# Optimization experiments

Measured on AMD Instinct MI355X. Metric: run time of the kernel, lower is better.

The kernel has to match this reference:

```python
import jax, jax.numpy as jnp
import numpy as np

ALPHA = 0.2
BETA = 1.0
TEMPERATURE = 0.05
EPS = 1e-8  # torch cosine_similarity eps


def setup_inputs() -> dict:
    key = jax.random.key(0)
    k1, k2 = jax.random.split(key)
    B, R, D = 4096, 18, 256  # rows, segment size (1 anchor + 1 pos + 16 negs), embed dim
    features = jax.random.normal(k1, (B * R, D), dtype=jnp.float32)
    scores = jax.random.normal(k2, (B * (R - 1),), dtype=jnp.float32)
    row_sizes = jnp.full((B,), R, dtype=jnp.int32)  # uniform ragged sizes
    logit_scale = jnp.array([1.0 / TEMPERATURE], dtype=jnp.float32)
    return {"features": features, "scores": scores, "row_sizes": row_sizes,
            "logit_scale": logit_scale}


def reference(features, scores, row_sizes, logit_scale):
    B = row_sizes.shape[0]
    R = features.shape[0] // B  # uniform segment size
    D = features.shape[1]
    f3 = features.reshape(B, R, D)
    anchor = f3[:, 0]          # [B, D]
    tgt = f3[:, 1:]            # [B, R-1, D]  (positive first, then negatives)

    # --- per-row cosine sims + log_softmax + KLDiv(batchmean) ---
    an = jnp.maximum(jnp.linalg.norm(anchor, axis=-1, keepdims=True), EPS)  # [B,1]
    tn = jnp.maximum(jnp.linalg.norm(tgt, axis=-1), EPS)                    # [B,R-1]
    cos = jnp.einsum('bd,bkd->bk', anchor, tgt) / (an * tn)                 # [B,R-1]
    emb_log = jax.nn.log_softmax(cos, axis=-1)                              # [B,R-1]
    ce = jax.nn.softmax(scores.reshape(B, R - 1), axis=-1)                  # [B,R-1]
    # torch KLDivLoss(reduction='batchmean') on a length-(R-1) vector divides by (R-1)
    kl = jnp.sum(ce * (jnp.log(ce) - emb_log), axis=-1) / (R - 1)           # [B]
    loss = jnp.mean(BETA * kl)

    # --- single InfoNCE over all rows: anchors vs [positives; all negatives] ---
    pos = f3[:, 1]                                   # [B, D]
    negs = f3[:, 2:].reshape(B * (R - 2), D)         # [B*(R-2), D]
    targets = jnp.concatenate([pos, negs], axis=0)   # [B*(R-1), D]
    logits = logit_scale[0] * (anchor @ targets.T)   # [B, B*(R-1)]
    labels = jnp.arange(B)
    # cross_entropy(logits, labels) with mean reduction
    infonce = jnp.mean(jax.nn.logsumexp(logits, axis=-1) - logits[labels, labels])

    return loss + ALPHA * infonce
```

## Files before the change

### kernel.cpp

```cpp
#include <hip/hip_runtime.h>
#include <math.h>

#define ALPHA 0.2f
#define BETA 1.0f
#define EPSV 1e-8f
#define LOG2E 1.4426950408889634f
#define LN2 0.6931471805599453f

#define BATCH 4096
#define RR 18
#define KT 17
#define DD 256
#define NTGT (BATCH*KT)

#define BMW 64
#define NWAVES 4
#define BMB (BMW*NWAVES)
#define MBLK (BATCH/BMB)
#define BN 64
#define NSPLIT 32
#define NSLOT (NSPLIT*2)
#define NSLICE (NTGT/NSPLIT)
#define NCHUNK (NSLICE/BN)
#define CHUNK_BYTES (BN*DD)
#define TSH_STRIDE 272

typedef int   i32x8  __attribute__((ext_vector_type(8)));
typedef float f32x16 __attribute__((ext_vector_type(16)));

__device__ inline void gl_lds16(const void* g, void* l){
  __builtin_amdgcn_global_load_lds(
      (const __attribute__((address_space(1))) unsigned int*)g,
      (__attribute__((address_space(3))) unsigned int*)l, 16, 0, 0);
}


__global__ __launch_bounds__(256) void prep_kernel(
    const float* __restrict__ feat, const float* __restrict__ scores,
    const float* __restrict__ lscale,
    unsigned char* __restrict__ abf8, unsigned char* __restrict__ tbf8,
    float* __restrict__ diag, float* __restrict__ klarr){
  __shared__ float csh[KT];
  __shared__ __align__(16) unsigned char tsh[KT*TSH_STRIDE];
  int b = blockIdx.x, tid = threadIdx.x, lane = tid & 63, wave = tid >> 6;
  const float* fb = feat + (size_t)b * RR * DD;
  float s2 = lscale[0] * LOG2E;

  float4 a4 = ((const float4*)fb)[lane];
  float asq = a4.x*a4.x + a4.y*a4.y + a4.z*a4.z + a4.w*a4.w;
  #pragma unroll
  for (int off=1; off<64; off<<=1) asq += __shfl_xor(asq, off);
  float an = fmaxf(sqrtf(asq), EPSV);

  if (wave == 0){
    int p = __builtin_amdgcn_cvt_pk_fp8_f32(a4.x*s2, a4.y*s2, 0, false);
    p     = __builtin_amdgcn_cvt_pk_fp8_f32(a4.z*s2, a4.w*s2, p, true);
    *(int*)(abf8 + (size_t)b*DD + lane*4) = p;
  }

  for (int kr = wave+1; kr <= KT; kr += NWAVES){
    float4 t4 = ((const float4*)(fb + (size_t)kr*DD))[lane];
    int p = __builtin_amdgcn_cvt_pk_fp8_f32(t4.x, t4.y, 0, false);
    p     = __builtin_amdgcn_cvt_pk_fp8_f32(t4.z, t4.w, p, true);
    *(int*)&tsh[(kr-1)*TSH_STRIDE + lane*4] = p;
    float d = a4.x*t4.x + a4.y*t4.y + a4.z*t4.z + a4.w*t4.w;
    float q = t4.x*t4.x + t4.y*t4.y + t4.z*t4.z + t4.w*t4.w;
    #pragma unroll
    for (int off=1; off<64; off<<=1){ d += __shfl_xor(d,off); q += __shfl_xor(q,off); }
    if (lane == 0){
      csh[kr-1] = d / (an * fmaxf(sqrtf(q), EPSV));
      if (kr == 1) diag[b] = d;
    }
  }
  __syncthreads();

  for (int idx = tid; idx < KT*16; idx += 256){
    int g = idx / KT;
    int j = idx - g*KT;
    int ki = g >> 2, half = (g >> 1) & 1, w = g & 1;
    int t  = b*KT + j;
    int c  = t >> 6, r = t & 63, mt = (r >> 5) & 1, m = r & 31;
    uint4 v = *(const uint4*)&tsh[j*TSH_STRIDE + ki*64 + half*32 + w*16];
    size_t dst = (size_t)c*CHUNK_BYTES + (size_t)((ki*2+mt)*2 + w)*1024
               + half*512 + m*16;
    *(uint4*)(tbf8 + dst) = v;
  }

  if (tid == 0){
    float cm = -INFINITY;
    #pragma unroll
    for (int j=0;j<KT;++j) cm = fmaxf(cm, csh[j]);
    float cs = 0.f;
    #pragma unroll
    for (int j=0;j<KT;++j) cs += __builtin_amdgcn_exp2f((csh[j]-cm)*LOG2E);
    float lse_c = cm + __logf(cs);

    const float* sb = scores + (size_t)b*KT;
    float sv[KT];
    #pragma unroll
    for (int j=0;j<KT;++j) sv[j] = sb[j];
    float sm = -INFINITY;
    #pragma unroll
    for (int j=0;j<KT;++j) sm = fmaxf(sm, sv[j]);
    float ss = 0.f;
    #pragma unroll
    for (int j=0;j<KT;++j) ss += __builtin_amdgcn_exp2f((sv[j]-sm)*LOG2E);
    float lse_s = sm + __logf(ss);

    float kl = 0.f;
    #pragma unroll
    for (int j=0;j<KT;++j){
      float lq = sv[j]  - lse_s;
      float lp = csh[j] - lse_c;
      kl += __builtin_amdgcn_exp2f(lq*LOG2E)*(lq - lp);
    }
    klarr[b] = kl * (1.0f/KT);
  }
}

__global__ __launch_bounds__(256,2) void gemm_lse_kernel(
    const unsigned char* __restrict__ abf8, const unsigned char* __restrict__ tbf8,
    float* __restrict__ part_m, float* __restrict__ part_s){
  __shared__ __align__(16) unsigned char Bs[2][CHUNK_BYTES];
  const int tid  = threadIdx.x;
  const int lane = tid & 63;
  const int wave = tid >> 6;
  const int mb   = blockIdx.y;
  const int ns   = blockIdx.x;
  const int l31  = lane & 31;
  const int half = lane >> 5;

  const char* gbase = (const char*)tbf8 + (size_t)(ns*NCHUNK)*CHUNK_BYTES;
  auto stage = [&](int ch){
    const char* g = gbase + (size_t)ch*CHUNK_BYTES;
    char* l = (char*)Bs[ch & 1];
    #pragma unroll
    for (int j=0;j<4;++j){
      int off = j*4096 + tid*16;
      gl_lds16(g + off, l + off);
    }
  };

  stage(0);

  i32x8 af[2][4];
  {
    const unsigned char* ab = abf8 + (size_t)(mb*BMB + wave*BMW)*DD;
    #pragma unroll
    for (int nt=0;nt<2;++nt)
      #pragma unroll
      for (int ki=0;ki<4;++ki){
        const unsigned char* p = ab + (size_t)(nt*32+l31)*DD + ki*64 + half*32;
        uint4 lo = *(const uint4*)p;
        uint4 hi = *(const uint4*)(p+16);
        af[nt][ki] = (i32x8){(int)lo.x,(int)lo.y,(int)lo.z,(int)lo.w,
                             (int)hi.x,(int)hi.y,(int)hi.z,(int)hi.w};
      }
  }

  float run_m[2] = {-INFINITY,-INFINITY};
  float run_s[2] = {0.f,0.f};

  for (int ch=0; ch<NCHUNK; ++ch){
    __syncthreads();
    if (ch+1 < NCHUNK) stage(ch+1);

    const unsigned char* frag = &Bs[ch & 1][0] + lane*16;

    f32x16 acc[2][2];
    #pragma unroll
    for (int mt=0;mt<2;++mt)
      #pragma unroll
      for (int nt=0;nt<2;++nt)
        acc[mt][nt] = (f32x16)(0.f);

    #pragma unroll
    for (int ki=0;ki<4;++ki){
      i32x8 tf[2];
      #pragma unroll
      for (int mt=0;mt<2;++mt){
        uint4 lo = *(const uint4*)(frag + (size_t)((ki*2+mt)*2+0)*1024);
        uint4 hi = *(const uint4*)(frag + (size_t)((ki*2+mt)*2+1)*1024);
        tf[mt] = (i32x8){(int)lo.x,(int)lo.y,(int)lo.z,(int)lo.w,
                         (int)hi.x,(int)hi.y,(int)hi.z,(int)hi.w};
      }
      acc[0][0] = __builtin_amdgcn_mfma_scale_f32_32x32x64_f8f6f4(
                      tf[0], af[0][ki], acc[0][0], 0,0, 0,127, 0,127);
      acc[0][1] = __builtin_amdgcn_mfma_scale_f32_32x32x64_f8f6f4(
                      tf[0], af[1][ki], acc[0][1], 0,0, 0,127, 0,127);
      acc[1][0] = __builtin_amdgcn_mfma_scale_f32_32x32x64_f8f6f4(
                      tf[1], af[0][ki], acc[1][0], 0,0, 0,127, 0,127);
      acc[1][1] = __builtin_amdgcn_mfma_scale_f32_32x32x64_f8f6f4(
                      tf[1], af[1][ki], acc[1][1], 0,0, 0,127, 0,127);
    }

    #pragma unroll
    for (int nt=0;nt<2;++nt){
      f32x16 t = __builtin_elementwise_max(acc[0][nt], acc[1][nt]);
      float m8[8];
      #pragma unroll
      for (int i=0;i<8;++i) m8[i] = fmaxf(t[i], t[i+8]);
      float m4a = fmaxf(m8[0],m8[1]), m4b = fmaxf(m8[2],m8[3]);
      float m4c = fmaxf(m8[4],m8[5]), m4d = fmaxf(m8[6],m8[7]);
      float mx = fmaxf(fmaxf(m4a,m4b), fmaxf(m4c,m4d));

      float s0=0.f, s1=0.f, s2=0.f, s3=0.f;
      #pragma unroll
      for (int r=0;r<16;r+=4){
        s0 += __builtin_amdgcn_exp2f(acc[0][nt][r  ]-mx) + __builtin_amdgcn_exp2f(acc[1][nt][r  ]-mx);
        s1 += __builtin_amdgcn_exp2f(acc[0][nt][r+1]-mx) + __builtin_amdgcn_exp2f(acc[1][nt][r+1]-mx);
        s2 += __builtin_amdgcn_exp2f(acc[0][nt][r+2]-mx) + __builtin_amdgcn_exp2f(acc[1][nt][r+2]-mx);
        s3 += __builtin_amdgcn_exp2f(acc[0][nt][r+3]-mx) + __builtin_amdgcn_exp2f(acc[1][nt][r+3]-mx);
      }
      float sh = (s0+s1)+(s2+s3);

      float nm = fmaxf(run_m[nt], mx);
      run_s[nt] = run_s[nt]*__builtin_amdgcn_exp2f(run_m[nt]-nm)
                + sh*__builtin_amdgcn_exp2f(mx-nm);
      run_m[nt] = nm;
    }
  }

  #pragma unroll
  for (int nt=0;nt<2;++nt){
    int gm = mb*BMB + wave*BMW + nt*32 + l31;
    int slot = ns*2 + half;
    part_m[(size_t)gm*NSLOT + slot] = run_m[nt];
    part_s[(size_t)gm*NSLOT + slot] = run_s[nt];
  }
}

__global__ __launch_bounds__(256) void combine_kernel(
    const float* __restrict__ part_m, const float* __restrict__ part_s,
    const float* __restrict__ diag, const float* __restrict__ klarr,
    const float* __restrict__ lscale, float* __restrict__ accs){
  int b = blockIdx.x*256 + threadIdx.x;
  float s = lscale[0];
  const float* pm = part_m + (size_t)b*NSLOT;
  const float* ps = part_s + (size_t)b*NSLOT;
  float M = -INFINITY;
  #pragma unroll 8
  for (int i=0;i<NSLOT;++i) M = fmaxf(M, pm[i]);
  float S = 0.f;
  #pragma unroll 8
  for (int i=0;i<NSLOT;++i) S += ps[i]*__builtin_amdgcn_exp2f(pm[i]-M);
  float inf = (M + __log2f(S))*LN2 - s*diag[b];
  float kl  = klarr[b];
  #pragma unroll
  for (int off=1; off<64; off<<=1){
    inf += __shfl_xor(inf, off);
    kl  += __shfl_xor(kl,  off);
  }
  if ((threadIdx.x & 63)==0){
    atomicAdd(accs+1, inf);
    atomicAdd(accs+0, kl);
  }
}

__global__ void final_kernel(const float* __restrict__ accs, float* __restrict__ out){
  out[0] = BETA*(accs[0]*(1.0f/BATCH)) + ALPHA*(accs[1]*(1.0f/BATCH));
}

extern "C" void kernel_launch(void* const* d_in, const int* in_sizes, int n_in,
                              void* d_out, int out_size, void* d_ws, size_t ws_size,
                              hipStream_t stream){
  const float* feat   = (const float*)d_in[0];
  const float* scores = (const float*)d_in[1];
  const float* lscale = (const float*)d_in[3];

  float* ws     = (float*)d_ws;
  float* diag   = ws;
  float* klarr  = diag + BATCH;
  float* part_m = klarr + BATCH;
  float* part_s = part_m + (size_t)BATCH*NSLOT;
  float* accs   = part_s + (size_t)BATCH*NSLOT;
  unsigned char* abf8 = (unsigned char*)(accs + 4);
  unsigned char* tbf8 = abf8 + (size_t)BATCH*DD;

  hipMemsetAsync(accs, 0, 2*sizeof(float), stream);
  prep_kernel<<<BATCH, 256, 0, stream>>>(feat, scores, lscale, abf8, tbf8, diag, klarr);
  gemm_lse_kernel<<<dim3(NSPLIT, MBLK), 256, 0, stream>>>(abf8, tbf8, part_m, part_s);
  combine_kernel<<<BATCH/256, 256, 0, stream>>>(part_m, part_s, diag, klarr, lscale, accs);
  final_kernel<<<1,1,0,stream>>>(accs, (float*)d_out);
}
```

Before: 216.6 us.

## Double GEMM split, drop LDS transpose in prep, wave-per-row combine, deterministic final reduce

The number of target-dimension splits in the fused GEMM+logsumexp kernel doubles to 64 and its occupancy hint rises to 3 blocks per CU, so the 16-row-block grid exposes more parallelism. The prep kernel now gives each 16-lane group one target row and writes the swizzled fp8 layout straight to global memory, dropping the shared-memory staging buffer and its extra pass. The combine step uses one wave per row with shuffle reductions over the larger set of partials, and a single-block final kernel replaces the memset and atomics. The risks are register pressure under the tighter launch bound and twice as much partial data for combine to read.

Measured after the change: 198.6 us. 8.3% less time.

```diff
diff --git a/kernel.cpp b/kernel.cpp
--- a/kernel.cpp
+++ b/kernel.cpp
@@ -18,12 +18,11 @@
 #define BMB (BMW*NWAVES)
 #define MBLK (BATCH/BMB)
 #define BN 64
-#define NSPLIT 32
+#define NSPLIT 64
 #define NSLOT (NSPLIT*2)
 #define NSLICE (NTGT/NSPLIT)
 #define NCHUNK (NSLICE/BN)
 #define CHUNK_BYTES (BN*DD)
-#define TSH_STRIDE 272
 
 typedef int   i32x8  __attribute__((ext_vector_type(8)));
 typedef float f32x16 __attribute__((ext_vector_type(16)));
@@ -32,6 +31,11 @@
   __builtin_amdgcn_global_load_lds(
       (const __attribute__((address_space(1))) unsigned int*)g,
       (__attribute__((address_space(3))) unsigned int*)l, 16, 0, 0);
+}
+
+__device__ inline int pk8(float a, float b, float c, float d){
+  int p = __builtin_amdgcn_cvt_pk_fp8_f32(a, b, 0, false);
+  return  __builtin_amdgcn_cvt_pk_fp8_f32(c, d, p, true);
 }
 
 
@@ -41,84 +45,93 @@
     unsigned char* __restrict__ abf8, unsigned char* __restrict__ tbf8,
     float* __restrict__ diag, float* __restrict__ klarr){
   __shared__ float csh[KT];
-  __shared__ __align__(16) unsigned char tsh[KT*TSH_STRIDE];
-  int b = blockIdx.x, tid = threadIdx.x, lane = tid & 63, wave = tid >> 6;
+  int b = blockIdx.x, tid = threadIdx.x;
+  int grp = tid >> 4, j = tid & 15;
   const float* fb = feat + (size_t)b * RR * DD;
   float s2 = lscale[0] * LOG2E;
 
-  float4 a4 = ((const float4*)fb)[lane];
-  float asq = a4.x*a4.x + a4.y*a4.y + a4.z*a4.z + a4.w*a4.w;
-  #pragma unroll
-  for (int off=1; off<64; off<<=1) asq += __shfl_xor(asq, off);
+  float4 a0 = ((const float4*)fb)[j*4+0];
+  float4 a1 = ((const float4*)fb)[j*4+1];
+  float4 a2 = ((const float4*)fb)[j*4+2];
+  float4 a3 = ((const float4*)fb)[j*4+3];
+  float asq = (a0.x*a0.x+a0.y*a0.y+a0.z*a0.z+a0.w*a0.w)
+            + (a1.x*a1.x+a1.y*a1.y+a1.z*a1.z+a1.w*a1.w)
+            + (a2.x*a2.x+a2.y*a2.y+a2.z*a2.z+a2.w*a2.w)
+            + (a3.x*a3.x+a3.y*a3.y+a3.z*a3.z+a3.w*a3.w);
+  #pragma unroll
+  for (int off=1; off<16; off<<=1) asq += __shfl_xor(asq, off);
   float an = fmaxf(sqrtf(asq), EPSV);
 
-  if (wave == 0){
-    int p = __builtin_amdgcn_cvt_pk_fp8_f32(a4.x*s2, a4.y*s2, 0, false);
-    p     = __builtin_amdgcn_cvt_pk_fp8_f32(a4.z*s2, a4.w*s2, p, true);
-    *(int*)(abf8 + (size_t)b*DD + lane*4) = p;
-  }
-
-  for (int kr = wave+1; kr <= KT; kr += NWAVES){
-    float4 t4 = ((const float4*)(fb + (size_t)kr*DD))[lane];
-    int p = __builtin_amdgcn_cvt_pk_fp8_f32(t4.x, t4.y, 0, false);
-    p     = __builtin_amdgcn_cvt_pk_fp8_f32(t4.z, t4.w, p, true);
-    *(int*)&tsh[(kr-1)*TSH_STRIDE + lane*4] = p;
-    float d = a4.x*t4.x + a4.y*t4.y + a4.z*t4.z + a4.w*t4.w;
-    float q = t4.x*t4.x + t4.y*t4.y + t4.z*t4.z + t4.w*t4.w;
-    #pragma unroll
-    for (int off=1; off<64; off<<=1){ d += __shfl_xor(d,off); q += __shfl_xor(q,off); }
-    if (lane == 0){
+  if (tid < 16){
+    uint4 v = make_uint4(
+      (unsigned)pk8(a0.x*s2,a0.y*s2,a0.z*s2,a0.w*s2),
+      (unsigned)pk8(a1.x*s2,a1.y*s2,a1.z*s2,a1.w*s2),
+      (unsigned)pk8(a2.x*s2,a2.y*s2,a2.z*s2,a2.w*s2),
+      (unsigned)pk8(a3.x*s2,a3.y*s2,a3.z*s2,a3.w*s2));
+    *(uint4*)(abf8 + (size_t)b*DD + j*16) = v;
+  }
+
+  for (int kr = grp+1; kr <= KT; kr += 16){
+    const float4* tp = (const float4*)(fb + (size_t)kr*DD) + j*4;
+    float4 t0=tp[0], t1=tp[1], t2=tp[2], t3=tp[3];
+    int t  = b*KT + (kr-1);
+    int c  = t >> 6, r = t & 63, mt = (r >> 5) & 1, m = r & 31;
+    int ki = j >> 2, hf = (j >> 1) & 1, w = j & 1;
+    uint4 v = make_uint4(
+      (unsigned)pk8(t0.x,t0.y,t0.z,t0.w), (unsigned)pk8(t1.x,t1.y,t1.z,t1.w),
+      (unsigned)pk8(t2.x,t2.y,t2.z,t2.w), (unsigned)pk8(t3.x,t3.y,t3.z,t3.w));
+    *(uint4*)(tbf8 + (size_t)c*CHUNK_BYTES + (size_t)((ki*2+mt)*2+w)*1024
+              + hf*512 + m*16) = v;
+    float d = (a0.x*t0.x+a0.y*t0.y+a0.z*t0.z+a0.w*t0.w)
+            + (a1.x*t1.x+a1.y*t1.y+a1.z*t1.z+a1.w*t1.w)
+            + (a2.x*t2.x+a2.y*t2.y+a2.z*t2.z+a2.w*t2.w)
+            + (a3.x*t3.x+a3.y*t3.y+a3.z*t3.z+a3.w*t3.w);
+    float q = (t0.x*t0.x+t0.y*t0.y+t0.z*t0.z+t0.w*t0.w)
+            + (t1.x*t1.x+t1.y*t1.y+t1.z*t1.z+t1.w*t1.w)
+            + (t2.x*t2.x+t2.y*t2.y+t2.z*t2.z+t2.w*t2.w)
+            + (t3.x*t3.x+t3.y*t3.y+t3.z*t3.z+t3.w*t3.w);
+    #pragma unroll
+    for (int off=1; off<16; off<<=1){ d += __shfl_xor(d,off); q += __shfl_xor(q,off); }
+    if (j == 0){
       csh[kr-1] = d / (an * fmaxf(sqrtf(q), EPSV));
       if (kr == 1) diag[b] = d;
     }
   }
   __syncthreads();
 
-  for (int idx = tid; idx < KT*16; idx += 256){
-    int g = idx / KT;
-    int j = idx - g*KT;
-    int ki = g >> 2, half = (g >> 1) & 1, w = g & 1;
-    int t  = b*KT + j;
-    int c  = t >> 6, r = t & 63, mt = (r >> 5) & 1, m = r & 31;
-    uint4 v = *(const uint4*)&tsh[j*TSH_STRIDE + ki*64 + half*32 + w*16];
-    size_t dst = (size_t)c*CHUNK_BYTES + (size_t)((ki*2+mt)*2 + w)*1024
-               + half*512 + m*16;
-    *(uint4*)(tbf8 + dst) = v;
-  }
-
   if (tid == 0){
     float cm = -INFINITY;
     #pragma unroll
-    for (int j=0;j<KT;++j) cm = fmaxf(cm, csh[j]);
+    for (int i=0;i<KT;++i) cm = fmaxf(cm, csh[i]);
     float cs = 0.f;
     #pragma unroll
-    for (int j=0;j<KT;++j) cs += __builtin_amdgcn_exp2f((csh[j]-cm)*LOG2E);
+    for (int i=0;i<KT;++i) cs += __builtin_amdgcn_exp2f((csh[i]-cm)*LOG2E);
     float lse_c = cm + __logf(cs);
 
     const float* sb = scores + (size_t)b*KT;
     float sv[KT];
     #pragma unroll
-    for (int j=0;j<KT;++j) sv[j] = sb[j];
+    for (int i=0;i<KT;++i) sv[i] = sb[i];
     float sm = -INFINITY;
     #pragma unroll
-    for (int j=0;j<KT;++j) sm = fmaxf(sm, sv[j]);
+    for (int i=0;i<KT;++i) sm = fmaxf(sm, sv[i]);
     float ss = 0.f;
     #pragma unroll
-    for (int j=0;j<KT;++j) ss += __builtin_amdgcn_exp2f((sv[j]-sm)*LOG2E);
+    for (int i=0;i<KT;++i) ss += __builtin_amdgcn_exp2f((sv[i]-sm)*LOG2E);
     float lse_s = sm + __logf(ss);
 
     float kl = 0.f;
     #pragma unroll
-    for (int j=0;j<KT;++j){
-      float lq = sv[j]  - lse_s;
-      float lp = csh[j] - lse_c;
+    for (int i=0;i<KT;++i){
+      float lq = sv[i]  - lse_s;
+      float lp = csh[i] - lse_c;
       kl += __builtin_amdgcn_exp2f(lq*LOG2E)*(lq - lp);
     }
     klarr[b] = kl * (1.0f/KT);
   }
 }
 
-__global__ __launch_bounds__(256,2) void gemm_lse_kernel(
+__global__ __launch_bounds__(256,3) void gemm_lse_kernel(
     const unsigned char* __restrict__ abf8, const unsigned char* __restrict__ tbf8,
     float* __restrict__ part_m, float* __restrict__ part_s){
   __shared__ __align__(16) unsigned char Bs[2][CHUNK_BYTES];
@@ -232,33 +245,44 @@
 
 __global__ __launch_bounds__(256) void combine_kernel(
     const float* __restrict__ part_m, const float* __restrict__ part_s,
-    const float* __restrict__ diag, const float* __restrict__ klarr,
-    const float* __restrict__ lscale, float* __restrict__ accs){
-  int b = blockIdx.x*256 + threadIdx.x;
+    const float* __restrict__ diag, const float* __restrict__ lscale,
+    float* __restrict__ infarr){
+  int lane = threadIdx.x & 63, wave = threadIdx.x >> 6;
+  int b = blockIdx.x*4 + wave;
   float s = lscale[0];
   const float* pm = part_m + (size_t)b*NSLOT;
   const float* ps = part_s + (size_t)b*NSLOT;
-  float M = -INFINITY;
-  #pragma unroll 8
-  for (int i=0;i<NSLOT;++i) M = fmaxf(M, pm[i]);
-  float S = 0.f;
-  #pragma unroll 8
-  for (int i=0;i<NSLOT;++i) S += ps[i]*__builtin_amdgcn_exp2f(pm[i]-M);
-  float inf = (M + __log2f(S))*LN2 - s*diag[b];
-  float kl  = klarr[b];
+  float m0 = pm[lane], m1 = pm[lane+64];
+  float v0 = ps[lane], v1 = ps[lane+64];
+  float M = fmaxf(m0, m1);
+  #pragma unroll
+  for (int off=1; off<64; off<<=1) M = fmaxf(M, __shfl_xor(M, off));
+  float S = v0*__builtin_amdgcn_exp2f(m0-M) + v1*__builtin_amdgcn_exp2f(m1-M);
+  #pragma unroll
+  for (int off=1; off<64; off<<=1) S += __shfl_xor(S, off);
+  if (lane == 0)
+    infarr[b] = (M + __log2f(S))*LN2 - s*diag[b];
+}
+
+__global__ __launch_bounds__(256) void final_kernel(
+    const float* __restrict__ infarr, const float* __restrict__ klarr,
+    float* __restrict__ out){
+  __shared__ float shi[4], shk[4];
+  int tid = threadIdx.x, lane = tid & 63, wave = tid >> 6;
+  float inf = 0.f, kl = 0.f;
+  for (int i = tid; i < BATCH; i += 256){ inf += infarr[i]; kl += klarr[i]; }
   #pragma unroll
   for (int off=1; off<64; off<<=1){
     inf += __shfl_xor(inf, off);
     kl  += __shfl_xor(kl,  off);
   }
-  if ((threadIdx.x & 63)==0){
-    atomicAdd(accs+1, inf);
-    atomicAdd(accs+0, kl);
-  }
-}
-
-__global__ void final_kernel(const float* __restrict__ accs, float* __restrict__ out){
-  out[0] = BETA*(accs[0]*(1.0f/BATCH)) + ALPHA*(accs[1]*(1.0f/BATCH));
+  if (lane == 0){ shi[wave] = inf; shk[wave] = kl; }
+  __syncthreads();
+  if (tid == 0){
+    float I = shi[0]+shi[1]+shi[2]+shi[3];
+    float K = shk[0]+shk[1]+shk[2]+shk[3];
+    out[0] = BETA*(K*(1.0f/BATCH)) + ALPHA*(I*(1.0f/BATCH));
+  }
 }
 
 extern "C" void kernel_launch(void* const* d_in, const int* in_sizes, int n_in,
@@ -271,15 +295,14 @@
   float* ws     = (float*)d_ws;
   float* diag   = ws;
   float* klarr  = diag + BATCH;
-  float* part_m = klarr + BATCH;
+  float* infarr = klarr + BATCH;
+  float* part_m = infarr + BATCH;
   float* part_s = part_m + (size_t)BATCH*NSLOT;
-  float* accs   = part_s + (size_t)BATCH*NSLOT;
-  unsigned char* abf8 = (unsigned char*)(accs + 4);
+  unsigned char* abf8 = (unsigned char*)(part_s + (size_t)BATCH*NSLOT);
   unsigned char* tbf8 = abf8 + (size_t)BATCH*DD;
 
-  hipMemsetAsync(accs, 0, 2*sizeof(float), stream);
   prep_kernel<<<BATCH, 256, 0, stream>>>(feat, scores, lscale, abf8, tbf8, diag, klarr);
   gemm_lse_kernel<<<dim3(NSPLIT, MBLK), 256, 0, stream>>>(abf8, tbf8, part_m, part_s);
-  combine_kernel<<<BATCH/256, 256, 0, stream>>>(part_m, part_s, diag, klarr, lscale, accs);
-  final_kernel<<<1,1,0,stream>>>(accs, (float*)d_out);
-}
+  combine_kernel<<<BATCH/4, 256, 0, stream>>>(part_m, part_s, diag, lscale, infarr);
+  final_kernel<<<1, 256, 0, stream>>>(infarr, klarr, (float*)d_out);
+}
```
